# Performance work log

Measured on AMD Instinct MI355X. Metric: run time of the kernel, lower is better.

The kernel has to match this reference:

```python
import jax, jax.numpy as jnp
import numpy as np

B, C, DM, H = 2, 256, 512, 8
D = DM // H          # d_head = 64
SPARSE_K = 64


def setup_inputs() -> dict:
    key = jax.random.key(0)
    ks = jax.random.split(key, 12)
    s = 0.02
    return {
        "x": jax.random.normal(ks[0], (B, C, DM), dtype=jnp.float32),
        "Wq": jax.random.normal(ks[1], (DM, DM), dtype=jnp.float32) * s,
        "bq": jnp.zeros((DM,), jnp.float32),
        "Wk": jax.random.normal(ks[2], (DM, DM), dtype=jnp.float32) * s,
        "bk": jnp.zeros((DM,), jnp.float32),
        "Wv": jax.random.normal(ks[3], (DM, DM), dtype=jnp.float32) * s,
        "bv": jnp.zeros((DM,), jnp.float32),
        "w1": jax.random.normal(ks[4], (D, 3 * D), dtype=jnp.float32) * s,
        "b1": jax.random.normal(ks[5], (D,), dtype=jnp.float32) * s,
        "w2": jax.random.normal(ks[6], (1, D), dtype=jnp.float32) * s,
        "b2": jax.random.normal(ks[7], (1,), dtype=jnp.float32) * s,
        "Wo": jax.random.normal(ks[8], (DM, DM), dtype=jnp.float32) * s,
        "bo": jnp.zeros((DM,), jnp.float32),
    }


def _heads(x, W, b):
    # torch Linear: x @ W.T + b, then (B,C,H,d) -> (B,H,C,d)
    y = jnp.einsum("bcD,ED->bcE", x, W) + b
    return y.reshape(B, C, H, D).transpose(0, 2, 1, 3)


def reference(x, Wq, bq, Wk, bk, Wv, bv, w1, b1, w2, b2, Wo, bo):
    q = _heads(x, Wq, bq)  # (B,H,C,d)
    k = _heads(x, Wk, bk)
    v = _heads(x, Wv, bv)

    # split first MLP layer weight: [:, :d] acts on q, [:, d:2d] on k, [:, 2d:] on q*k
    q_p = jnp.einsum("bhcd,ed->bhce", q, w1[:, :D])
    k_p = jnp.einsum("bhcd,ed->bhce", k, w1[:, D:2 * D])

    # res: (B,H,C,C,d)
    res = q_p[:, :, :, None, :] + k_p[:, :, None, :, :] + b1
    interaction = q[:, :, :, None, :] * k[:, :, None, :, :]
    res = res + jnp.einsum("bhije,fe->bhijf", interaction, w1[:, 2 * D:])

    # second MLP layer -> scalar score per pair, exact (erf) GELU as torch default
    h = jax.nn.gelu(res, approximate=False)
    scores = (jnp.einsum("bhijd,od->bhijo", h, w2) + b2)[..., 0]
    scores = scores / jnp.sqrt(jnp.float32(D))

    if SPARSE_K < C:
        top_vals = jax.lax.top_k(scores, SPARSE_K)[0]
        thresh = top_vals[..., -1:]
        scores = jnp.where(scores >= thresh, scores, jnp.float32(-1e9))

    attn = jax.nn.softmax(scores, axis=-1)  # dropout is identity (p=0 / eval)
    out = jnp.einsum("bhij,bhjd->bhid", attn, v)
    out = out.transpose(0, 2, 1, 3).reshape(B, C, DM)
    return jnp.einsum("bcD,ED->bcE", out, Wo) + bo
```

## Files before the change

kernel.cpp:

```cpp
#include <hip/hip_runtime.h>
#include <math.h>

typedef __bf16 bf16;
typedef __attribute__((ext_vector_type(4))) __bf16 bf16x4;
typedef __attribute__((ext_vector_type(8))) __bf16 bf16x8;
typedef __attribute__((ext_vector_type(4))) float floatx4;

__device__ __forceinline__ float gelu_exact(float x) {
    float tt = x * 0.70710678118654752440f;
    float e;
    if (__builtin_expect(fabsf(tt) > 0.5f, 0)) {
        e = erff(tt);
    } else {
        float s = tt * tt;
        e = tt * fmaf(s, fmaf(s, fmaf(s, fmaf(s, fmaf(s,
                -8.548327023450852e-4f, 5.223977625442188e-3f),
                -2.6866170645131252e-2f), 0.11283791670955126f),
                -0.3761263890318375f), 1.1283791670955126f);
    }
    return 0.5f * x * (1.0f + e);
}

__device__ __forceinline__ void split3(float a, bf16& h, bf16& m, bf16& l) {
    h = (bf16)a;  float r1 = a - (float)h;
    m = (bf16)r1; float r2 = r1 - (float)m;
    l = (bf16)r2;
}

struct SplitArgs {
    const float* src[5];
    bf16* h[5]; bf16* m[5]; bf16* l[5];
};

__global__ __launch_bounds__(256) void split3_512_kernel(SplitArgs S) {
    int z = blockIdx.z;
    const float* src = S.src[z];
    bf16* dh = S.h[z]; bf16* dm = S.m[z]; bf16* dl = S.l[z];
    int t = blockIdx.x * 256 + threadIdx.x;
    int row = t >> 7, kq = (t & 127) * 4;
    int rt = row >> 4, rm = row & 15;
    int ks = kq >> 5, q4 = (kq >> 3) & 3, u0 = kq & 7;
    int dst = ((rt * 16 + ks) * 64 + q4 * 16 + rm) * 8 + u0;
    float4 vv = *(const float4*)&src[row * 512 + kq];
    float a4[4] = {vv.x, vv.y, vv.z, vv.w};
    bf16x4 h, m, l;
    #pragma unroll
    for (int u = 0; u < 4; u++) {
        bf16 hh, mm, ll;
        split3(a4[u], hh, mm, ll);
        h[u] = hh; m[u] = mm; l[u] = ll;
    }
    *(bf16x4*)&dh[dst] = h;
    *(bf16x4*)&dm[dst] = m;
    *(bf16x4*)&dl[dst] = l;
}

struct MM2Args {
    const bf16 *Ah, *Am, *Al;
    const bf16 *Wh[3], *Wm[3], *Wl[3];
    const float* bias[3];
    float* outf[3];
    bf16 *kh, *km, *kl;
    int mode[3];
};

__global__ __launch_bounds__(64) void mm_mfma_kernel(MM2Args A) {
    const int z = blockIdx.z;
    const bf16* Wh = A.Wh[z]; const bf16* Wm = A.Wm[z]; const bf16* Wl = A.Wl[z];
    const float* bias = A.bias[z];
    const int lane = threadIdx.x;
    const int m16 = lane & 15, q4 = lane >> 4;
    const int mt = blockIdx.y, bx = blockIdx.x;

    floatx4 acc;
    {
        float bv = bias[bx * 16 + m16];
        acc[0] = bv; acc[1] = bv; acc[2] = bv; acc[3] = bv;
    }

    #pragma unroll 4
    for (int ks = 0; ks < 16; ks++) {
        int sa = ((mt * 16 + ks) * 64 + lane) * 8;
        bf16x8 ah = *(const bf16x8*)&A.Ah[sa];
        bf16x8 am = *(const bf16x8*)&A.Am[sa];
        bf16x8 al = *(const bf16x8*)&A.Al[sa];
        int sw = ((bx * 16 + ks) * 64 + lane) * 8;
        bf16x8 wh = *(const bf16x8*)&Wh[sw];
        bf16x8 wm = *(const bf16x8*)&Wm[sw];
        bf16x8 wl = *(const bf16x8*)&Wl[sw];
        acc = __builtin_amdgcn_mfma_f32_16x16x32_bf16(ah, wh, acc, 0, 0, 0);
        acc = __builtin_amdgcn_mfma_f32_16x16x32_bf16(ah, wm, acc, 0, 0, 0);
        acc = __builtin_amdgcn_mfma_f32_16x16x32_bf16(am, wh, acc, 0, 0, 0);
        acc = __builtin_amdgcn_mfma_f32_16x16x32_bf16(ah, wl, acc, 0, 0, 0);
        acc = __builtin_amdgcn_mfma_f32_16x16x32_bf16(al, wh, acc, 0, 0, 0);
        acc = __builtin_amdgcn_mfma_f32_16x16x32_bf16(am, wm, acc, 0, 0, 0);
    }

    const int mode = A.mode[z];
    const int n = bx * 16 + m16;
    #pragma unroll
    for (int r = 0; r < 4; r++) {
        int m = mt * 16 + q4 * 4 + r;
        float val = acc[r];
        if (mode == 0) {
            A.outf[z][m * 512 + n] = val;
        } else if (mode == 1) {
            A.outf[z][(((m >> 8) * 8 + (n >> 6)) * 256 + (m & 255)) * 64 + (n & 63)] = val;
        } else {
            int krow = ((m >> 8) * 8 + (n >> 6)) * 256 + (m & 255);
            int d = n & 63;
            int dst = (((krow >> 4) * 2 + (d >> 5)) * 64 + ((d >> 3) & 3) * 16 + (krow & 15)) * 8 + (d & 7);
            bf16 h, mm, l;
            split3(val, h, mm, l);
            A.kh[dst] = h; A.km[dst] = mm; A.kl[dst] = l;
        }
    }
}

__global__ __launch_bounds__(256, 3) void fused_mfma_attn_kernel(
    const float* __restrict__ q, const float* __restrict__ v,
    const bf16* __restrict__ khi, const bf16* __restrict__ kmid, const bf16* __restrict__ klo,
    const float* __restrict__ w1, const float* __restrict__ b1,
    const float* __restrict__ w2, const float* __restrict__ b2,
    bf16* __restrict__ oh, bf16* __restrict__ om, bf16* __restrict__ ol)
{
    const int i2 = blockIdx.x;
    const int bh = blockIdx.y;
    const int t  = threadIdx.x;
    const int lane = t & 63, w = t >> 6;
    const int m16 = lane & 15, q4 = lane >> 4;

    __shared__ float part[2][4][256];
    __shared__ float sc[2][256];
    __shared__ float qpb_s[2][64];
    __shared__ float sbuf[2][256];
    __shared__ float red[2][4][64];
    __shared__ float red2[2][4];
    __shared__ float thr_s[2], smax_s[2];

    const int f = w * 16 + m16;
    const float* w1row = w1 + f * 192;

    bf16x8 Ah[2][2], Am[2][2], Al[2][2];
    #pragma unroll
    for (int i01 = 0; i01 < 2; i01++) {
        const float* qrow = q + (bh * 256 + i2 * 2 + i01) * 64;
        float qa = 0.f;
        #pragma unroll
        for (int ks = 0; ks < 2; ks++) {
            int e0 = ks * 32 + q4 * 8;
            #pragma unroll
            for (int u = 0; u < 2; u++) {
                int e = e0 + u * 4;
                float4 wa = *(const float4*)&w1row[e];
                float4 wb = *(const float4*)&w1row[64 + e];
                float4 wc = *(const float4*)&w1row[128 + e];
                float4 qv = *(const float4*)&qrow[e];
                qa += wa.x * qv.x + wa.y * qv.y + wa.z * qv.z + wa.w * qv.w;
                float av[4];
                av[0] = fmaf(wc.x, qv.x, wb.x);
                av[1] = fmaf(wc.y, qv.y, wb.y);
                av[2] = fmaf(wc.z, qv.z, wb.z);
                av[3] = fmaf(wc.w, qv.w, wb.w);
                #pragma unroll
                for (int uu = 0; uu < 4; uu++) {
                    bf16 h, m, l;
                    split3(av[uu], h, m, l);
                    Ah[i01][ks][u * 4 + uu] = h;
                    Am[i01][ks][u * 4 + uu] = m;
                    Al[i01][ks][u * 4 + uu] = l;
                }
            }
        }
        qa += __shfl_xor(qa, 16);
        qa += __shfl_xor(qa, 32);
        if (lane < 16) qpb_s[i01][w * 16 + lane] = qa + b1[w * 16 + lane];
    }
    __syncthreads();

    floatx4 qpbr[2];
    qpbr[0] = *(const floatx4*)&qpb_s[0][w * 16 + q4 * 4];
    qpbr[1] = *(const floatx4*)&qpb_s[1][w * 16 + q4 * 4];
    const float4 w2f = *(const float4*)&w2[w * 16 + q4 * 4];
    const float b2v = b2[0];

    #pragma unroll 2
    for (int jt = 0; jt < 16; jt++) {
        int base = ((bh * 16 + jt) * 2 * 64 + lane) * 8;
        bf16x8 Kh0 = *(const bf16x8*)&khi [base];
        bf16x8 Km0 = *(const bf16x8*)&kmid[base];
        bf16x8 Kl0 = *(const bf16x8*)&klo [base];
        bf16x8 Kh1 = *(const bf16x8*)&khi [base + 512];
        bf16x8 Km1 = *(const bf16x8*)&kmid[base + 512];
        bf16x8 Kl1 = *(const bf16x8*)&klo [base + 512];
        #pragma unroll
        for (int i01 = 0; i01 < 2; i01++) {
            floatx4 a = qpbr[i01];
            a = __builtin_amdgcn_mfma_f32_16x16x32_bf16(Ah[i01][0], Kh0, a, 0, 0, 0);
            a = __builtin_amdgcn_mfma_f32_16x16x32_bf16(Ah[i01][0], Km0, a, 0, 0, 0);
            a = __builtin_amdgcn_mfma_f32_16x16x32_bf16(Am[i01][0], Kh0, a, 0, 0, 0);
            a = __builtin_amdgcn_mfma_f32_16x16x32_bf16(Ah[i01][0], Kl0, a, 0, 0, 0);
            a = __builtin_amdgcn_mfma_f32_16x16x32_bf16(Al[i01][0], Kh0, a, 0, 0, 0);
            a = __builtin_amdgcn_mfma_f32_16x16x32_bf16(Am[i01][0], Km0, a, 0, 0, 0);
            a = __builtin_amdgcn_mfma_f32_16x16x32_bf16(Ah[i01][1], Kh1, a, 0, 0, 0);
            a = __builtin_amdgcn_mfma_f32_16x16x32_bf16(Ah[i01][1], Km1, a, 0, 0, 0);
            a = __builtin_amdgcn_mfma_f32_16x16x32_bf16(Am[i01][1], Kh1, a, 0, 0, 0);
            a = __builtin_amdgcn_mfma_f32_16x16x32_bf16(Ah[i01][1], Kl1, a, 0, 0, 0);
            a = __builtin_amdgcn_mfma_f32_16x16x32_bf16(Al[i01][1], Kh1, a, 0, 0, 0);
            a = __builtin_amdgcn_mfma_f32_16x16x32_bf16(Am[i01][1], Km1, a, 0, 0, 0);
            float s = 0.f;
            s = fmaf(w2f.x, gelu_exact(a[0]), s);
            s = fmaf(w2f.y, gelu_exact(a[1]), s);
            s = fmaf(w2f.z, gelu_exact(a[2]), s);
            s = fmaf(w2f.w, gelu_exact(a[3]), s);
            s += __shfl_xor(s, 16);
            s += __shfl_xor(s, 32);
            if (lane < 16) part[i01][w][jt * 16 + lane] = s;
        }
    }
    __syncthreads();

    float score[2];
    #pragma unroll
    for (int i01 = 0; i01 < 2; i01++) {
        score[i01] = (((part[i01][0][t] + part[i01][1][t]) +
                       (part[i01][2][t] + part[i01][3][t])) + b2v) * 0.125f;
    }

    float sv0 = score[0], sv1 = score[1];
    #pragma unroll
    for (int k = 2; k <= 256; k <<= 1) {
        #pragma unroll
        for (int j = k >> 1; j >= 1; j >>= 1) {
            float pv0, pv1;
            if (j >= 64) {
                sbuf[0][t] = sv0; sbuf[1][t] = sv1;
                __syncthreads();
                pv0 = sbuf[0][t ^ j]; pv1 = sbuf[1][t ^ j];
                __syncthreads();
            } else {
                pv0 = __shfl_xor(sv0, j);
                pv1 = __shfl_xor(sv1, j);
            }
            bool keepMin = (((t & j) == 0) == ((t & k) == 0));
            sv0 = keepMin ? fminf(sv0, pv0) : fmaxf(sv0, pv0);
            sv1 = keepMin ? fminf(sv1, pv1) : fmaxf(sv1, pv1);
        }
    }
    if (t == 192) { thr_s[0] = sv0; thr_s[1] = sv1; }
    if (t == 255) { smax_s[0] = sv0; smax_s[1] = sv1; }
    __syncthreads();

    float p0 = (score[0] >= thr_s[0]) ? __expf(score[0] - smax_s[0]) : 0.0f;
    float p1 = (score[1] >= thr_s[1]) ? __expf(score[1] - smax_s[1]) : 0.0f;
    sc[0][t] = p0; sc[1][t] = p1;
    float ps0 = p0, ps1 = p1;
    #pragma unroll
    for (int mask = 1; mask < 64; mask <<= 1) {
        ps0 += __shfl_xor(ps0, mask);
        ps1 += __shfl_xor(ps1, mask);
    }
    if (lane == 0) { red2[0][w] = ps0; red2[1][w] = ps1; }
    __syncthreads();
    const float inv0 = 1.0f / ((red2[0][0] + red2[0][1]) + (red2[0][2] + red2[0][3]));
    const float inv1 = 1.0f / ((red2[1][0] + red2[1][1]) + (red2[1][2] + red2[1][3]));

    const int d = t & 63, g = t >> 6;
    const float* vb = v + bh * 256 * 64;
    float a0 = 0.f, a1 = 0.f;
    for (int j4 = 0; j4 < 16; j4++) {
        int jj = g * 64 + j4 * 4;
        float4 p40 = *(const float4*)&sc[0][jj];
        float4 p41 = *(const float4*)&sc[1][jj];
        float v0 = vb[(jj + 0) * 64 + d];
        float v1 = vb[(jj + 1) * 64 + d];
        float v2 = vb[(jj + 2) * 64 + d];
        float v3 = vb[(jj + 3) * 64 + d];
        a0 = fmaf(p40.x, v0, a0); a1 = fmaf(p41.x, v0, a1);
        a0 = fmaf(p40.y, v1, a0); a1 = fmaf(p41.y, v1, a1);
        a0 = fmaf(p40.z, v2, a0); a1 = fmaf(p41.z, v2, a1);
        a0 = fmaf(p40.w, v3, a0); a1 = fmaf(p41.w, v3, a1);
    }
    red[0][g][d] = a0; red[1][g][d] = a1;
    __syncthreads();

    if (t < 128) {
        int i01 = t >> 6, dd = t & 63;
        float o = ((red[i01][0][dd] + red[i01][1][dd]) +
                   (red[i01][2][dd] + red[i01][3][dd])) * (i01 ? inv1 : inv0);
        int b = bh >> 3, h = bh & 7;
        int row = b * 256 + i2 * 2 + i01;
        int n = h * 64 + dd;
        int dst = (((row >> 4) * 16 + (n >> 5)) * 64 + ((n >> 3) & 3) * 16 + (row & 15)) * 8 + (n & 7);
        bf16 hh, mm, ll;
        split3(o, hh, mm, ll);
        oh[dst] = hh; om[dst] = mm; ol[dst] = ll;
    }
}

extern "C" void kernel_launch(void* const* d_in, const int* in_sizes, int n_in,
                              void* d_out, int out_size, void* d_ws, size_t ws_size,
                              hipStream_t stream) {
    const float* x  = (const float*)d_in[0];
    const float* Wq = (const float*)d_in[1];
    const float* bq = (const float*)d_in[2];
    const float* Wk = (const float*)d_in[3];
    const float* bk = (const float*)d_in[4];
    const float* Wv = (const float*)d_in[5];
    const float* bv = (const float*)d_in[6];
    const float* w1 = (const float*)d_in[7];
    const float* b1 = (const float*)d_in[8];
    const float* w2 = (const float*)d_in[9];
    const float* b2 = (const float*)d_in[10];
    const float* Wo = (const float*)d_in[11];
    const float* bo = (const float*)d_in[12];
    float* out = (float*)d_out;

    const int NE = 262144;
    float* qb  = (float*)d_ws;
    float* vb  = qb + NE;
    bf16* base = (bf16*)(vb + NE);
    bf16* khi  = base;            bf16* kmid = khi + NE;    bf16* klo = kmid + NE;
    bf16* xs   = klo + NE;
    bf16* wqs  = xs  + 3 * NE;
    bf16* wks  = wqs + 3 * NE;
    bf16* wvs  = wks + 3 * NE;
    bf16* wos  = wvs + 3 * NE;
    bf16* oas  = wos + 3 * NE;

    {
        SplitArgs S;
        const float* srcs[5] = {x, Wq, Wk, Wv, Wo};
        bf16* dsts[5] = {xs, wqs, wks, wvs, wos};
        for (int z = 0; z < 5; z++) {
            S.src[z] = srcs[z];
            S.h[z] = dsts[z]; S.m[z] = dsts[z] + NE; S.l[z] = dsts[z] + 2 * NE;
        }
        split3_512_kernel<<<dim3(256, 1, 5), 256, 0, stream>>>(S);
    }
    {
        MM2Args M;
        M.Ah = xs; M.Am = xs + NE; M.Al = xs + 2 * NE;
        M.Wh[0] = wqs; M.Wm[0] = wqs + NE; M.Wl[0] = wqs + 2 * NE;
        M.Wh[1] = wks; M.Wm[1] = wks + NE; M.Wl[1] = wks + 2 * NE;
        M.Wh[2] = wvs; M.Wm[2] = wvs + NE; M.Wl[2] = wvs + 2 * NE;
        M.bias[0] = bq; M.bias[1] = bk; M.bias[2] = bv;
        M.outf[0] = qb; M.outf[1] = nullptr; M.outf[2] = vb;
        M.kh = khi; M.km = kmid; M.kl = klo;
        M.mode[0] = 1; M.mode[1] = 2; M.mode[2] = 1;
        mm_mfma_kernel<<<dim3(32, 32, 3), 64, 0, stream>>>(M);
    }
    fused_mfma_attn_kernel<<<dim3(128, 16), 256, 0, stream>>>(
        qb, vb, khi, kmid, klo, w1, b1, w2, b2,
        oas, oas + NE, oas + 2 * NE);
    {
        MM2Args M;
        M.Ah = oas; M.Am = oas + NE; M.Al = oas + 2 * NE;
        M.Wh[0] = wos; M.Wm[0] = wos + NE; M.Wl[0] = wos + 2 * NE;
        M.Wh[1] = wos; M.Wm[1] = wos; M.Wl[1] = wos;
        M.Wh[2] = wos; M.Wm[2] = wos; M.Wl[2] = wos;
        M.bias[0] = bo; M.bias[1] = bo; M.bias[2] = bo;
        M.outf[0] = out; M.outf[1] = out; M.outf[2] = out;
        M.kh = khi; M.km = kmid; M.kl = klo;
        M.mode[0] = 0; M.mode[1] = 0; M.mode[2] = 0;
        mm_mfma_kernel<<<dim3(32, 32, 1), 64, 0, stream>>>(M);
    }
}
```

Before: 182.5 us.

## Fuse bf16 triple-split into GEMM loads and drop separate split kernel

Removes the standalone split3 kernel that pre-converted x and the weights into hi/mid/lo bf16 layouts. The GEMM kernel now loads fp32 rows directly and splits them in registers before the MFMAs. The attention kernel writes plain fp32 output instead of split bf16. This saves one launch and the extra global write/read traffic, at the cost of redundant split arithmetic per tile and less coalesced fp32 row loads.

```diff
diff --git a/kernel.cpp b/kernel.cpp
--- a/kernel.cpp
+++ b/kernel.cpp
@@ -27,47 +27,28 @@
     l = (bf16)r2;
 }
 
-struct SplitArgs {
-    const float* src[5];
-    bf16* h[5]; bf16* m[5]; bf16* l[5];
-};
-
-__global__ __launch_bounds__(256) void split3_512_kernel(SplitArgs S) {
-    int z = blockIdx.z;
-    const float* src = S.src[z];
-    bf16* dh = S.h[z]; bf16* dm = S.m[z]; bf16* dl = S.l[z];
-    int t = blockIdx.x * 256 + threadIdx.x;
-    int row = t >> 7, kq = (t & 127) * 4;
-    int rt = row >> 4, rm = row & 15;
-    int ks = kq >> 5, q4 = (kq >> 3) & 3, u0 = kq & 7;
-    int dst = ((rt * 16 + ks) * 64 + q4 * 16 + rm) * 8 + u0;
-    float4 vv = *(const float4*)&src[row * 512 + kq];
-    float a4[4] = {vv.x, vv.y, vv.z, vv.w};
-    bf16x4 h, m, l;
-    #pragma unroll
-    for (int u = 0; u < 4; u++) {
+__device__ __forceinline__ void split8(const float* v, bf16x8& h, bf16x8& m, bf16x8& l) {
+    #pragma unroll
+    for (int u = 0; u < 8; u++) {
         bf16 hh, mm, ll;
-        split3(a4[u], hh, mm, ll);
+        split3(v[u], hh, mm, ll);
         h[u] = hh; m[u] = mm; l[u] = ll;
     }
-    *(bf16x4*)&dh[dst] = h;
-    *(bf16x4*)&dm[dst] = m;
-    *(bf16x4*)&dl[dst] = l;
-}
-
-struct MM2Args {
-    const bf16 *Ah, *Am, *Al;
-    const bf16 *Wh[3], *Wm[3], *Wl[3];
+}
+
+struct MM3Args {
+    const float* A;
+    const float* W[3];
     const float* bias[3];
     float* outf[3];
     bf16 *kh, *km, *kl;
     int mode[3];
 };
 
-__global__ __launch_bounds__(64) void mm_mfma_kernel(MM2Args A) {
+__global__ __launch_bounds__(64) void mm_fp32_mfma_kernel(MM3Args P) {
     const int z = blockIdx.z;
-    const bf16* Wh = A.Wh[z]; const bf16* Wm = A.Wm[z]; const bf16* Wl = A.Wl[z];
-    const float* bias = A.bias[z];
+    const float* W = P.W[z];
+    const float* bias = P.bias[z];
     const int lane = threadIdx.x;
     const int m16 = lane & 15, q4 = lane >> 4;
     const int mt = blockIdx.y, bx = blockIdx.x;
@@ -78,16 +59,19 @@
         acc[0] = bv; acc[1] = bv; acc[2] = bv; acc[3] = bv;
     }
 
+    const float* arow = P.A + (mt * 16 + m16) * 512 + q4 * 8;
+    const float* wrow = W   + (bx * 16 + m16) * 512 + q4 * 8;
+
     #pragma unroll 4
     for (int ks = 0; ks < 16; ks++) {
-        int sa = ((mt * 16 + ks) * 64 + lane) * 8;
-        bf16x8 ah = *(const bf16x8*)&A.Ah[sa];
-        bf16x8 am = *(const bf16x8*)&A.Am[sa];
-        bf16x8 al = *(const bf16x8*)&A.Al[sa];
-        int sw = ((bx * 16 + ks) * 64 + lane) * 8;
-        bf16x8 wh = *(const bf16x8*)&Wh[sw];
-        bf16x8 wm = *(const bf16x8*)&Wm[sw];
-        bf16x8 wl = *(const bf16x8*)&Wl[sw];
+        float av[8], wv[8];
+        *(float4*)&av[0] = *(const float4*)&arow[ks * 32];
+        *(float4*)&av[4] = *(const float4*)&arow[ks * 32 + 4];
+        *(float4*)&wv[0] = *(const float4*)&wrow[ks * 32];
+        *(float4*)&wv[4] = *(const float4*)&wrow[ks * 32 + 4];
+        bf16x8 ah, am, al, wh, wm, wl;
+        split8(av, ah, am, al);
+        split8(wv, wh, wm, wl);
         acc = __builtin_amdgcn_mfma_f32_16x16x32_bf16(ah, wh, acc, 0, 0, 0);
         acc = __builtin_amdgcn_mfma_f32_16x16x32_bf16(ah, wm, acc, 0, 0, 0);
         acc = __builtin_amdgcn_mfma_f32_16x16x32_bf16(am, wh, acc, 0, 0, 0);
@@ -96,23 +80,23 @@
         acc = __builtin_amdgcn_mfma_f32_16x16x32_bf16(am, wm, acc, 0, 0, 0);
     }
 
-    const int mode = A.mode[z];
+    const int mode = P.mode[z];
     const int n = bx * 16 + m16;
     #pragma unroll
     for (int r = 0; r < 4; r++) {
         int m = mt * 16 + q4 * 4 + r;
         float val = acc[r];
         if (mode == 0) {
-            A.outf[z][m * 512 + n] = val;
+            P.outf[z][m * 512 + n] = val;
         } else if (mode == 1) {
-            A.outf[z][(((m >> 8) * 8 + (n >> 6)) * 256 + (m & 255)) * 64 + (n & 63)] = val;
+            P.outf[z][(((m >> 8) * 8 + (n >> 6)) * 256 + (m & 255)) * 64 + (n & 63)] = val;
         } else {
             int krow = ((m >> 8) * 8 + (n >> 6)) * 256 + (m & 255);
             int d = n & 63;
             int dst = (((krow >> 4) * 2 + (d >> 5)) * 64 + ((d >> 3) & 3) * 16 + (krow & 15)) * 8 + (d & 7);
             bf16 h, mm, l;
             split3(val, h, mm, l);
-            A.kh[dst] = h; A.km[dst] = mm; A.kl[dst] = l;
+            P.kh[dst] = h; P.km[dst] = mm; P.kl[dst] = l;
         }
     }
 }
@@ -122,7 +106,7 @@
     const bf16* __restrict__ khi, const bf16* __restrict__ kmid, const bf16* __restrict__ klo,
     const float* __restrict__ w1, const float* __restrict__ b1,
     const float* __restrict__ w2, const float* __restrict__ b2,
-    bf16* __restrict__ oh, bf16* __restrict__ om, bf16* __restrict__ ol)
+    float* __restrict__ oa)
 {
     const int i2 = blockIdx.x;
     const int bh = blockIdx.y;
@@ -290,11 +274,7 @@
                    (red[i01][2][dd] + red[i01][3][dd])) * (i01 ? inv1 : inv0);
         int b = bh >> 3, h = bh & 7;
         int row = b * 256 + i2 * 2 + i01;
-        int n = h * 64 + dd;
-        int dst = (((row >> 4) * 16 + (n >> 5)) * 64 + ((n >> 3) & 3) * 16 + (row & 15)) * 8 + (n & 7);
-        bf16 hh, mm, ll;
-        split3(o, hh, mm, ll);
-        oh[dst] = hh; om[dst] = mm; ol[dst] = ll;
+        oa[row * 512 + h * 64 + dd] = o;
     }
 }
 
@@ -317,52 +297,33 @@
     float* out = (float*)d_out;
 
     const int NE = 262144;
-    float* qb  = (float*)d_ws;
-    float* vb  = qb + NE;
-    bf16* base = (bf16*)(vb + NE);
-    bf16* khi  = base;            bf16* kmid = khi + NE;    bf16* klo = kmid + NE;
-    bf16* xs   = klo + NE;
-    bf16* wqs  = xs  + 3 * NE;
-    bf16* wks  = wqs + 3 * NE;
-    bf16* wvs  = wks + 3 * NE;
-    bf16* wos  = wvs + 3 * NE;
-    bf16* oas  = wos + 3 * NE;
+    float* qb = (float*)d_ws;
+    float* vb = qb + NE;
+    float* oa = vb + NE;
+    bf16* khi  = (bf16*)(oa + NE);
+    bf16* kmid = khi + NE;
+    bf16* klo  = kmid + NE;
 
     {
-        SplitArgs S;
-        const float* srcs[5] = {x, Wq, Wk, Wv, Wo};
-        bf16* dsts[5] = {xs, wqs, wks, wvs, wos};
-        for (int z = 0; z < 5; z++) {
-            S.src[z] = srcs[z];
-            S.h[z] = dsts[z]; S.m[z] = dsts[z] + NE; S.l[z] = dsts[z] + 2 * NE;
-        }
-        split3_512_kernel<<<dim3(256, 1, 5), 256, 0, stream>>>(S);
-    }
-    {
-        MM2Args M;
-        M.Ah = xs; M.Am = xs + NE; M.Al = xs + 2 * NE;
-        M.Wh[0] = wqs; M.Wm[0] = wqs + NE; M.Wl[0] = wqs + 2 * NE;
-        M.Wh[1] = wks; M.Wm[1] = wks + NE; M.Wl[1] = wks + 2 * NE;
-        M.Wh[2] = wvs; M.Wm[2] = wvs + NE; M.Wl[2] = wvs + 2 * NE;
+        MM3Args M;
+        M.A = x;
+        M.W[0] = Wq; M.W[1] = Wk; M.W[2] = Wv;
         M.bias[0] = bq; M.bias[1] = bk; M.bias[2] = bv;
         M.outf[0] = qb; M.outf[1] = nullptr; M.outf[2] = vb;
         M.kh = khi; M.km = kmid; M.kl = klo;
         M.mode[0] = 1; M.mode[1] = 2; M.mode[2] = 1;
-        mm_mfma_kernel<<<dim3(32, 32, 3), 64, 0, stream>>>(M);
+        mm_fp32_mfma_kernel<<<dim3(32, 32, 3), 64, 0, stream>>>(M);
     }
     fused_mfma_attn_kernel<<<dim3(128, 16), 256, 0, stream>>>(
-        qb, vb, khi, kmid, klo, w1, b1, w2, b2,
-        oas, oas + NE, oas + 2 * NE);
+        qb, vb, khi, kmid, klo, w1, b1, w2, b2, oa);
     {
-        MM2Args M;
-        M.Ah = oas; M.Am = oas + NE; M.Al = oas + 2 * NE;
-        M.Wh[0] = wos; M.Wm[0] = wos + NE; M.Wl[0] = wos + 2 * NE;
-        M.Wh[1] = wos; M.Wm[1] = wos; M.Wl[1] = wos;
-        M.Wh[2] = wos; M.Wm[2] = wos; M.Wl[2] = wos;
+        MM3Args M;
+        M.A = oa;
+        M.W[0] = Wo; M.W[1] = Wo; M.W[2] = Wo;
         M.bias[0] = bo; M.bias[1] = bo; M.bias[2] = bo;
         M.outf[0] = out; M.outf[1] = out; M.outf[2] = out;
         M.kh = khi; M.km = kmid; M.kl = klo;
         M.mode[0] = 0; M.mode[1] = 0; M.mode[2] = 0;
-        mm_mfma_kernel<<<dim3(32, 32, 1), 64, 0, stream>>>(M);
-    }
-}
+        mm_fp32_mfma_kernel<<<dim3(32, 32, 1), 64, 0, stream>>>(M);
+    }
+}
```

New measurement: 190.9 us. +4.6%, slower.
